# Kernel optimization log

Measured on AMD Instinct MI355X. Metric: run time of the kernel, lower is better.

The kernel has to match this reference:

```python
import jax, jax.numpy as jnp
import numpy as np

DIM = 256
FOCAL_LEVEL = 3
FOCAL_WINDOW = 3
FOCAL_FACTOR = 2


def _dwconv(x, k):
    # depthwise conv, SAME padding via explicit k//2 (matches ZeroPadding2D + VALID Conv2D)
    p = k.shape[0] // 2
    return jax.lax.conv_general_dilated(
        x, k, window_strides=(1, 1), padding=[(p, p), (p, p)],
        dimension_numbers=("NHWC", "HWIO", "NHWC"), feature_group_count=DIM)


def setup_inputs() -> dict:
    key = jax.random.key(0)
    ks = jax.random.split(key, 8)
    B, H, W = 32, 64, 64
    C_out = 2 * DIM + (FOCAL_LEVEL + 1)  # 516
    x = jax.random.normal(ks[0], (B, H, W, DIM), jnp.float32)
    w_init = jax.random.normal(ks[1], (DIM, C_out), jnp.float32) * 0.02
    b_init = jnp.zeros((C_out,), jnp.float32)
    kernels = []
    for i in range(FOCAL_LEVEL):
        s = FOCAL_FACTOR * i + FOCAL_WINDOW  # 3, 5, 7
        kernels.append(jax.random.normal(ks[2 + i], (s, s, 1, DIM), jnp.float32) * 0.02)
    w_mod = jax.random.normal(ks[5], (DIM, DIM), jnp.float32) * 0.02
    b_mod = jnp.zeros((DIM,), jnp.float32)
    w_proj = jax.random.normal(ks[6], (DIM, DIM), jnp.float32) * 0.02
    b_proj = jnp.zeros((DIM,), jnp.float32)
    return {"x": x, "w_init": w_init, "b_init": b_init,
            "k0": kernels[0], "k1": kernels[1], "k2": kernels[2],
            "w_mod": w_mod, "b_mod": b_mod, "w_proj": w_proj, "b_proj": b_proj}


def reference(x, w_init, b_init, k0, k1, k2, w_mod, b_mod, w_proj, b_proj):
    gelu = lambda t: jax.nn.gelu(t, approximate=False)
    x_proj = x @ w_init + b_init                       # [B,H,W,2*DIM+L+1]
    query = x_proj[..., :DIM]
    context = x_proj[..., DIM:2 * DIM]
    gates = jnp.clip(x_proj[..., 2 * DIM:], -1.0, 1.0)  # [B,H,W,L+1]

    ctx = gelu(_dwconv(context, k0))
    context_all = ctx * gates[..., 0:1]
    for idx, k in enumerate((k1, k2), start=1):
        ctx = gelu(_dwconv(ctx, k))
        context_all = context_all + ctx * gates[..., idx:idx + 1]

    context_global = jnp.tanh(jnp.mean(ctx, axis=(1, 2), keepdims=True))  # GAP+tanh
    context_all = context_all + context_global * gates[..., FOCAL_LEVEL:]

    modulator = context_all @ w_mod + b_mod            # 1x1 conv == per-pixel dense
    query = jnp.clip(query, -100.0, 100.0)
    modulator = jnp.clip(modulator, -100.0, 100.0)
    out = (query * modulator) @ w_proj + b_proj        # dropout identity (eval)
    return out
```

## Files before the change

### kernel.cpp

```cpp
#include <hip/hip_runtime.h>
#include <math.h>

#define DIMC 256
#define CO   516
#define NB   32
#define NH   64
#define NW   64
#define NPIX (NB*NH*NW)
#define PITCH 264
#define CP    76
#define CROWS 72

typedef short short8 __attribute__((ext_vector_type(8)));
typedef float floatx4 __attribute__((ext_vector_type(4)));
typedef unsigned short us4 __attribute__((ext_vector_type(4)));

__device__ __forceinline__ float gelu_f(float x) {
    return 0.5f * x * (1.0f + erff(x * 0.7071067811865476f));
}
__device__ __forceinline__ float clip100(float v) {
    return fminf(100.f, fmaxf(-100.f, v));
}
__device__ __forceinline__ void split2(float x, unsigned short& h, unsigned short& l) {
    unsigned int xb = __float_as_uint(x);
    unsigned int hb = (xb + 0x7fffu + ((xb >> 16) & 1u)) & 0xffff0000u;
    h = (unsigned short)(hb >> 16);
    float r = x - __uint_as_float(hb);
    unsigned int rb = __float_as_uint(r);
    l = (unsigned short)((rb + 0x7fffu + ((rb >> 16) & 1u)) >> 16);
}

__global__ __launch_bounds__(256) void k_prep(const float* __restrict__ w_init,
                                              const float* __restrict__ w_mod,
                                              const float* __restrict__ w_proj,
                                              unsigned short* wiF_h, unsigned short* wiF_l,
                                              unsigned short* wmF_h, unsigned short* wmF_l,
                                              unsigned short* wpF_h, unsigned short* wpF_l,
                                              unsigned short* wgF_h, unsigned short* wgF_l) {
    const int n = blockIdx.x;
    const int k = threadIdx.x;
    const int kki = k >> 5, quad = (k >> 3) & 3, j = k & 7;
    unsigned short h, l;
    if (n < 1024) {
        const int nn = (n < 512) ? n : (n < 768 ? n - 512 : n - 768);
        const int g = nn >> 6, in_ = (nn >> 4) & 3, l15 = nn & 15;
        const size_t idx = ((size_t)((g * 8 + kki) * 4 + in_) * 64 + quad * 16 + l15) * 8 + j;
        if (n < 512) {
            split2(w_init[k * CO + n], h, l);
            wiF_h[idx] = h; wiF_l[idx] = l;
        } else if (n < 768) {
            split2(w_mod[k * 256 + nn], h, l);
            wmF_h[idx] = h; wmF_l[idx] = l;
        } else {
            split2(w_proj[k * 256 + nn], h, l);
            wpF_h[idx] = h; wpF_l[idx] = l;
        }
    } else {
        const int nn = n - 1024;
        const float v = (nn < 4) ? w_init[k * CO + 512 + nn] : 0.f;
        split2(v, h, l);
        const size_t idx = ((size_t)kki * 64 + quad * 16 + nn) * 8 + j;
        wgF_h[idx] = h; wgF_l[idx] = l;
    }
}

__global__ __launch_bounds__(256) void k_init_mfma(const float* __restrict__ x,
                                                   const unsigned short* __restrict__ wiF_h,
                                                   const unsigned short* __restrict__ wiF_l,
                                                   const unsigned short* __restrict__ wgF_h,
                                                   const unsigned short* __restrict__ wgF_l,
                                                   const float* __restrict__ b_init,
                                                   float* __restrict__ qout,
                                                   float* __restrict__ ctxp,
                                                   float* __restrict__ gates) {
    __shared__ unsigned short Ah[8192];
    __shared__ unsigned short Al[8192];
    const int t = threadIdx.x;
    const int wv = t >> 6, lane = t & 63;
    const int l15 = lane & 15, quad = lane >> 4;
    const long tile = blockIdx.x;
    const long p0 = tile * 64;
    const int bb = (int)(p0 >> 12);
    const int pl = (int)(p0 & 4095);

    const float* xr = x + (size_t)(p0 + wv * 16 + l15) * 256 + quad * 8;
    const unsigned short* BqH = wiF_h + (size_t)wv * 16384;
    const unsigned short* BqL = wiF_l + (size_t)wv * 16384;
    const unsigned short* BcH = wiF_h + (size_t)(4 + wv) * 16384;
    const unsigned short* BcL = wiF_l + (size_t)(4 + wv) * 16384;

    floatx4 accq[4][4], accc[4][4], gacc;
    #pragma unroll
    for (int im = 0; im < 4; ++im)
        #pragma unroll
        for (int in_ = 0; in_ < 4; ++in_) {
            accq[im][in_] = (floatx4){0.f, 0.f, 0.f, 0.f};
            accc[im][in_] = (floatx4){0.f, 0.f, 0.f, 0.f};
        }
    gacc = (floatx4){0.f, 0.f, 0.f, 0.f};

    #pragma unroll
    for (int h = 0; h < 2; ++h) {
        #pragma unroll
        for (int kk2 = 0; kk2 < 4; ++kk2) {
            const int kki = h * 4 + kk2;
            const float4 v0 = *(const float4*)&xr[kki * 32];
            const float4 v1 = *(const float4*)&xr[kki * 32 + 4];
            short8 hh, ll;
            unsigned short hs, ls;
            split2(v0.x, hs, ls); hh[0] = (short)hs; ll[0] = (short)ls;
            split2(v0.y, hs, ls); hh[1] = (short)hs; ll[1] = (short)ls;
            split2(v0.z, hs, ls); hh[2] = (short)hs; ll[2] = (short)ls;
            split2(v0.w, hs, ls); hh[3] = (short)hs; ll[3] = (short)ls;
            split2(v1.x, hs, ls); hh[4] = (short)hs; ll[4] = (short)ls;
            split2(v1.y, hs, ls); hh[5] = (short)hs; ll[5] = (short)ls;
            split2(v1.z, hs, ls); hh[6] = (short)hs; ll[6] = (short)ls;
            split2(v1.w, hs, ls); hh[7] = (short)hs; ll[7] = (short)ls;
            const int o = ((wv * 4 + kk2) * 64 + lane) * 8;
            *(short8*)&Ah[o] = hh;
            *(short8*)&Al[o] = ll;
        }
        __syncthreads();

        #pragma unroll
        for (int kk2 = 0; kk2 < 4; ++kk2) {
            const int kki = h * 4 + kk2;
            short8 ah[4], al[4], bh[4], bl[4];
            #pragma unroll
            for (int im = 0; im < 4; ++im) {
                const int o = ((im * 4 + kk2) * 64 + lane) * 8;
                ah[im] = *(const short8*)&Ah[o];
                al[im] = *(const short8*)&Al[o];
            }
            #pragma unroll
            for (int in_ = 0; in_ < 4; ++in_) {
                const int o = ((kki * 4 + in_) * 64 + lane) * 8;
                bh[in_] = *(const short8*)&BqH[o];
                bl[in_] = *(const short8*)&BqL[o];
            }
            #pragma unroll
            for (int im = 0; im < 4; ++im)
                #pragma unroll
                for (int in_ = 0; in_ < 4; ++in_) {
                    accq[im][in_] = __builtin_amdgcn_mfma_f32_16x16x32_bf16(ah[im], bh[in_], accq[im][in_], 0, 0, 0);
                    accq[im][in_] = __builtin_amdgcn_mfma_f32_16x16x32_bf16(ah[im], bl[in_], accq[im][in_], 0, 0, 0);
                    accq[im][in_] = __builtin_amdgcn_mfma_f32_16x16x32_bf16(al[im], bh[in_], accq[im][in_], 0, 0, 0);
                }
            #pragma unroll
            for (int in_ = 0; in_ < 4; ++in_) {
                const int o = ((kki * 4 + in_) * 64 + lane) * 8;
                bh[in_] = *(const short8*)&BcH[o];
                bl[in_] = *(const short8*)&BcL[o];
            }
            #pragma unroll
            for (int im = 0; im < 4; ++im)
                #pragma unroll
                for (int in_ = 0; in_ < 4; ++in_) {
                    accc[im][in_] = __builtin_amdgcn_mfma_f32_16x16x32_bf16(ah[im], bh[in_], accc[im][in_], 0, 0, 0);
                    accc[im][in_] = __builtin_amdgcn_mfma_f32_16x16x32_bf16(ah[im], bl[in_], accc[im][in_], 0, 0, 0);
                    accc[im][in_] = __builtin_amdgcn_mfma_f32_16x16x32_bf16(al[im], bh[in_], accc[im][in_], 0, 0, 0);
                }
            {
                const int oga = ((wv * 4 + kk2) * 64 + lane) * 8;
                const short8 gah = *(const short8*)&Ah[oga];
                const short8 gal = *(const short8*)&Al[oga];
                const int ob = (kki * 64 + lane) * 8;
                const short8 gbh = *(const short8*)&wgF_h[ob];
                const short8 gbl = *(const short8*)&wgF_l[ob];
                gacc = __builtin_amdgcn_mfma_f32_16x16x32_bf16(gah, gbh, gacc, 0, 0, 0);
                gacc = __builtin_amdgcn_mfma_f32_16x16x32_bf16(gah, gbl, gacc, 0, 0, 0);
                gacc = __builtin_amdgcn_mfma_f32_16x16x32_bf16(gal, gbh, gacc, 0, 0, 0);
            }
        }
        if (h == 0) __syncthreads();
    }

    #pragma unroll
    for (int in_ = 0; in_ < 4; ++in_) {
        const int col = wv * 64 + in_ * 16 + l15;
        const float bi = b_init[col];
        #pragma unroll
        for (int im = 0; im < 4; ++im)
            #pragma unroll
            for (int r = 0; r < 4; ++r) {
                const int row = im * 16 + quad * 4 + r;
                qout[(p0 + row) * 256 + col] = accq[im][in_][r] + bi;
            }
    }
    #pragma unroll
    for (int in_ = 0; in_ < 4; ++in_) {
        const int col = wv * 64 + in_ * 16 + l15;
        const float bi = b_init[256 + col];
        #pragma unroll
        for (int im = 0; im < 4; ++im) {
            float4 o;
            o.x = accc[im][in_][0] + bi;
            o.y = accc[im][in_][1] + bi;
            o.z = accc[im][in_][2] + bi;
            o.w = accc[im][in_][3] + bi;
            *(float4*)&ctxp[((size_t)bb * 256 + col) * 4096 + pl + im * 16 + quad * 4] = o;
        }
    }
    if (l15 < 4) {
        const float bi = b_init[512 + l15];
        #pragma unroll
        for (int r = 0; r < 4; ++r) {
            const int row = wv * 16 + quad * 4 + r;
            gates[(p0 + row) * 4 + l15] = fminf(1.f, fmaxf(-1.f, gacc[r] + bi));
        }
    }
}

template<int KS>
__device__ __forceinline__ void conv_level(const float* __restrict__ kwp,
                                           const float* __restrict__ I,
                                           int ry0, int cx0, float v[8]) {
    constexpr int P = KS / 2;
    constexpr int RWIN = 2 + 2 * P;
    float wk[KS * KS];
    #pragma unroll
    for (int i = 0; i < KS * KS; ++i) wk[i] = kwp[i * 256];

    float4 rb[RWIN][3];
    #pragma unroll
    for (int r = 0; r < 2 * P; ++r) {
        const int base = (ry0 + r - P + 4) * CP + cx0;
        rb[r][0] = *(const float4*)&I[base];
        rb[r][1] = *(const float4*)&I[base + 4];
        rb[r][2] = *(const float4*)&I[base + 8];
    }
    #pragma unroll
    for (int j = 0; j < 2; ++j) {
        {
            const int r = j + 2 * P;
            const int base = (ry0 + r - P + 4) * CP + cx0;
            rb[r][0] = *(const float4*)&I[base];
            rb[r][1] = *(const float4*)&I[base + 4];
            rb[r][2] = *(const float4*)&I[base + 8];
        }
        float s0 = 0.f, s1 = 0.f, s2 = 0.f, s3 = 0.f;
        #pragma unroll
        for (int dy = 0; dy < KS; ++dy) {
            const float* rw = (const float*)&rb[j + dy][0];
            #pragma unroll
            for (int dx = 0; dx < KS; ++dx) {
                const float wgt = wk[dy * KS + dx];
                s0 += rw[4 - P + 0 + dx] * wgt;
                s1 += rw[4 - P + 1 + dx] * wgt;
                s2 += rw[4 - P + 2 + dx] * wgt;
                s3 += rw[4 - P + 3 + dx] * wgt;
            }
        }
        v[j * 4 + 0] = gelu_f(s0);
        v[j * 4 + 1] = gelu_f(s1);
        v[j * 4 + 2] = gelu_f(s2);
        v[j * 4 + 3] = gelu_f(s3);
    }
}

__global__ __launch_bounds__(512) void k_conv_fused(const float* __restrict__ ctxp,
                                                    const float* __restrict__ k0,
                                                    const float* __restrict__ k1,
                                                    const float* __restrict__ k2,
                                                    const float* __restrict__ gates,
                                                    float* __restrict__ c_allp) {
    __shared__ float X[CROWS * CP];
    __shared__ float Y[CROWS * CP];
    const int t = threadIdx.x;
    const int bc = blockIdx.x;
    const int b = bc >> 8, c = bc & 255;
    const float* src = ctxp + (size_t)bc * 4096;

    for (int i = t; i < CROWS * CP; i += 512) { X[i] = 0.f; Y[i] = 0.f; }
    __syncthreads();
    #pragma unroll
    for (int i = 0; i < 2; ++i) {
        const int p = i * 2048 + t * 4;
        const float4 vv = *(const float4*)&src[p];
        *(float4*)&X[((p >> 6) + 4) * CP + (p & 63) + 4] = vv;
    }
    __syncthreads();

    const int px = t & 15, py = t >> 4;
    const int cx0 = px * 4, ry0 = py * 2;
    const float* gbase = gates + (size_t)b * 4096 * 4;

    float acc[8], v[8];

    conv_level<3>(k0 + c, X, ry0, cx0, v);
    #pragma unroll
    for (int j = 0; j < 2; ++j) {
        *(float4*)&Y[(ry0 + j + 4) * CP + cx0 + 4] = *(float4*)&v[j * 4];
        #pragma unroll
        for (int i2 = 0; i2 < 4; ++i2)
            acc[j * 4 + i2] = v[j * 4 + i2] * gbase[((ry0 + j) * 64 + cx0 + i2) * 4 + 0];
    }
    __syncthreads();

    conv_level<5>(k1 + c, Y, ry0, cx0, v);
    #pragma unroll
    for (int j = 0; j < 2; ++j) {
        *(float4*)&X[(ry0 + j + 4) * CP + cx0 + 4] = *(float4*)&v[j * 4];
        #pragma unroll
        for (int i2 = 0; i2 < 4; ++i2)
            acc[j * 4 + i2] += v[j * 4 + i2] * gbase[((ry0 + j) * 64 + cx0 + i2) * 4 + 1];
    }
    __syncthreads();

    conv_level<7>(k2 + c, X, ry0, cx0, v);
    float vsum = 0.f;
    #pragma unroll
    for (int j = 0; j < 2; ++j)
        #pragma unroll
        for (int i2 = 0; i2 < 4; ++i2) {
            acc[j * 4 + i2] += v[j * 4 + i2] * gbase[((ry0 + j) * 64 + cx0 + i2) * 4 + 2];
            vsum += v[j * 4 + i2];
        }

    __syncthreads();
    X[t] = vsum;
    __syncthreads();
    if (t < 64) {
        float s = 0.f;
        #pragma unroll
        for (int k = 0; k < 8; ++k) s += X[t + 64 * k];
        #pragma unroll
        for (int off = 32; off >= 1; off >>= 1)
            s += __shfl_down(s, off, 64);
        if (t == 0) X[0] = tanhf(s * (1.f / 4096.f));
    }
    __syncthreads();
    const float gl = X[0];

    float* dst = c_allp + (size_t)bc * 4096;
    #pragma unroll
    for (int j = 0; j < 2; ++j) {
        float4 o;
        o.x = acc[j * 4 + 0] + gl * gbase[((ry0 + j) * 64 + cx0 + 0) * 4 + 3];
        o.y = acc[j * 4 + 1] + gl * gbase[((ry0 + j) * 64 + cx0 + 1) * 4 + 3];
        o.z = acc[j * 4 + 2] + gl * gbase[((ry0 + j) * 64 + cx0 + 2) * 4 + 3];
        o.w = acc[j * 4 + 3] + gl * gbase[((ry0 + j) * 64 + cx0 + 3) * 4 + 3];
        *(float4*)&dst[(ry0 + j) * 64 + cx0] = o;
    }
}

__global__ __launch_bounds__(256) void k_final_mfma(float* qout,
                                                    const float* __restrict__ c_allp,
                                                    const unsigned short* __restrict__ wmF_h,
                                                    const unsigned short* __restrict__ wmF_l,
                                                    const unsigned short* __restrict__ wpF_h,
                                                    const unsigned short* __restrict__ wpF_l,
                                                    const float* __restrict__ b_mod,
                                                    const float* __restrict__ b_proj) {
    __shared__ unsigned short Ah[64 * PITCH];
    __shared__ unsigned short Al[64 * PITCH];
    const int t = threadIdx.x;
    const long p0 = (long)blockIdx.x * 64;
    const int b = (int)(p0 >> 12);
    const int pl = (int)(p0 & 4095);

    {
        const float* src = c_allp + ((size_t)b * 256 + t) * 4096 + pl;
        #pragma unroll
        for (int i = 0; i < 16; ++i) {
            const float4 vv = *(const float4*)&src[i * 4];
            unsigned short h, l;
            split2(vv.x, h, l); Ah[(i*4+0)*PITCH + t] = h; Al[(i*4+0)*PITCH + t] = l;
            split2(vv.y, h, l); Ah[(i*4+1)*PITCH + t] = h; Al[(i*4+1)*PITCH + t] = l;
            split2(vv.z, h, l); Ah[(i*4+2)*PITCH + t] = h; Al[(i*4+2)*PITCH + t] = l;
            split2(vv.w, h, l); Ah[(i*4+3)*PITCH + t] = h; Al[(i*4+3)*PITCH + t] = l;
        }
    }
    __syncthreads();

    const int wv = t >> 6, lane = t & 63;
    const int l15 = lane & 15, quad = lane >> 4;
    const int ncol0 = wv * 64;
    const unsigned short* BmH = wmF_h + (size_t)wv * 16384;
    const unsigned short* BmL = wmF_l + (size_t)wv * 16384;
    const unsigned short* BpH = wpF_h + (size_t)wv * 16384;
    const unsigned short* BpL = wpF_l + (size_t)wv * 16384;

    floatx4 acc[4][4];
    #pragma unroll
    for (int im = 0; im < 4; ++im)
        #pragma unroll
        for (int in_ = 0; in_ < 4; ++in_)
            acc[im][in_] = (floatx4){0.f, 0.f, 0.f, 0.f};

    #pragma unroll
    for (int kki = 0; kki < 8; ++kki) {
        short8 ah[4], al[4], bh[4], bl[4];
        #pragma unroll
        for (int in_ = 0; in_ < 4; ++in_) {
            const int o = ((kki * 4 + in_) * 64 + lane) * 8;
            bh[in_] = *(const short8*)&BmH[o];
            bl[in_] = *(const short8*)&BmL[o];
        }
        #pragma unroll
        for (int im = 0; im < 4; ++im) {
            const int off = (im * 16 + l15) * PITCH + kki * 32 + quad * 8;
            ah[im] = *(const short8*)&Ah[off];
            al[im] = *(const short8*)&Al[off];
        }
        #pragma unroll
        for (int im = 0; im < 4; ++im)
            #pragma unroll
            for (int in_ = 0; in_ < 4; ++in_) {
                acc[im][in_] = __builtin_amdgcn_mfma_f32_16x16x32_bf16(ah[im], bh[in_], acc[im][in_], 0, 0, 0);
                acc[im][in_] = __builtin_amdgcn_mfma_f32_16x16x32_bf16(ah[im], bl[in_], acc[im][in_], 0, 0, 0);
                acc[im][in_] = __builtin_amdgcn_mfma_f32_16x16x32_bf16(al[im], bh[in_], acc[im][in_], 0, 0, 0);
            }
    }
    __syncthreads();

    #pragma unroll
    for (int in_ = 0; in_ < 4; ++in_) {
        const int col = ncol0 + in_ * 16 + l15;
        const float bm = b_mod[col];
        #pragma unroll
        for (int im = 0; im < 4; ++im)
            #pragma unroll
            for (int r = 0; r < 4; ++r) {
                const int row = im * 16 + quad * 4 + r;
                const float m = clip100(acc[im][in_][r] + bm);
                const float qv = clip100(qout[(p0 + row) * 256 + col]);
                unsigned short h, l;
                split2(qv * m, h, l);
                Ah[row * PITCH + col] = h;
                Al[row * PITCH + col] = l;
            }
    }
    __syncthreads();

    #pragma unroll
    for (int im = 0; im < 4; ++im)
        #pragma unroll
        for (int in_ = 0; in_ < 4; ++in_)
            acc[im][in_] = (floatx4){0.f, 0.f, 0.f, 0.f};

    #pragma unroll
    for (int kki = 0; kki < 8; ++kki) {
        short8 ah[4], al[4], bh[4], bl[4];
        #pragma unroll
        for (int in_ = 0; in_ < 4; ++in_) {
            const int o = ((kki * 4 + in_) * 64 + lane) * 8;
            bh[in_] = *(const short8*)&BpH[o];
            bl[in_] = *(const short8*)&BpL[o];
        }
        #pragma unroll
        for (int im = 0; im < 4; ++im) {
            const int off = (im * 16 + l15) * PITCH + kki * 32 + quad * 8;
            ah[im] = *(const short8*)&Ah[off];
            al[im] = *(const short8*)&Al[off];
        }
        #pragma unroll
        for (int im = 0; im < 4; ++im)
            #pragma unroll
            for (int in_ = 0; in_ < 4; ++in_) {
                acc[im][in_] = __builtin_amdgcn_mfma_f32_16x16x32_bf16(ah[im], bh[in_], acc[im][in_], 0, 0, 0);
                acc[im][in_] = __builtin_amdgcn_mfma_f32_16x16x32_bf16(ah[im], bl[in_], acc[im][in_], 0, 0, 0);
                acc[im][in_] = __builtin_amdgcn_mfma_f32_16x16x32_bf16(al[im], bh[in_], acc[im][in_], 0, 0, 0);
            }
    }

    #pragma unroll
    for (int in_ = 0; in_ < 4; ++in_) {
        const int col = ncol0 + in_ * 16 + l15;
        const float bp = b_proj[col];
        #pragma unroll
        for (int im = 0; im < 4; ++im)
            #pragma unroll
            for (int r = 0; r < 4; ++r) {
                const int row = im * 16 + quad * 4 + r;
                qout[(p0 + row) * 256 + col] = acc[im][in_][r] + bp;
            }
    }
}

extern "C" void kernel_launch(void* const* d_in, const int* in_sizes, int n_in,
                              void* d_out, int out_size, void* d_ws, size_t ws_size,
                              hipStream_t stream) {
    const float* x      = (const float*)d_in[0];
    const float* w_init = (const float*)d_in[1];
    const float* b_init = (const float*)d_in[2];
    const float* k0     = (const float*)d_in[3];
    const float* k1     = (const float*)d_in[4];
    const float* k2     = (const float*)d_in[5];
    const float* w_mod  = (const float*)d_in[6];
    const float* b_mod  = (const float*)d_in[7];
    const float* w_proj = (const float*)d_in[8];
    const float* b_proj = (const float*)d_in[9];
    float* qout = (float*)d_out;

    float* ws = (float*)d_ws;
    const long NP = (long)NPIX * DIMC;
    float* ctxp    = ws;
    float* c_allp  = ws + NP;
    float* gates   = ws + 2 * NP;
    unsigned short* wiF_h = (unsigned short*)(gates + (long)NPIX * 4);
    unsigned short* wiF_l = wiF_h + 512 * 256;
    unsigned short* wmF_h = wiF_l + 512 * 256;
    unsigned short* wmF_l = wmF_h + 256 * 256;
    unsigned short* wpF_h = wmF_l + 256 * 256;
    unsigned short* wpF_l = wpF_h + 256 * 256;
    unsigned short* wgF_h = wpF_l + 256 * 256;
    unsigned short* wgF_l = wgF_h + 16 * 256;

    k_prep<<<1040, 256, 0, stream>>>(w_init, w_mod, w_proj,
                                     wiF_h, wiF_l, wmF_h, wmF_l, wpF_h, wpF_l,
                                     wgF_h, wgF_l);
    k_init_mfma<<<NPIX / 64, 256, 0, stream>>>(x, wiF_h, wiF_l,
                                               wgF_h, wgF_l, b_init,
                                               qout, ctxp, gates);
    k_conv_fused<<<NB * 256, 512, 0, stream>>>(ctxp, k0, k1, k2, gates, c_allp);
    k_final_mfma<<<NPIX / 64, 256, 0, stream>>>(qout, c_allp,
                                                wmF_h, wmF_l, wpF_h, wpF_l,
                                                b_mod, b_proj);
}
```

Measured before the change: 866.0 us.

## Store gates planar per batch, stream conv rows, zero only halo

Gates are now written in a planar [B,4,H*W] layout, so the depthwise conv kernel reads them as coalesced float4 loads instead of strided scalar loads. The conv inner routine streams each input row once and accumulates both output rows from it, which removes the register row buffer and the preloaded weight array. Only the halo border of the shared buffers is zeroed, and a separate small shared array is used for the reduction. Weights are now reloaded from global memory inside the loop, which adds redundant loads that may or may not be served from cache.

Result: faster. 836.7 us (-3.4%).

```diff
diff --git a/kernel.cpp b/kernel.cpp
--- a/kernel.cpp
+++ b/kernel.cpp
@@ -13,7 +13,6 @@
 
 typedef short short8 __attribute__((ext_vector_type(8)));
 typedef float floatx4 __attribute__((ext_vector_type(4)));
-typedef unsigned short us4 __attribute__((ext_vector_type(4)));
 
 __device__ __forceinline__ float gelu_f(float x) {
     return 0.5f * x * (1.0f + erff(x * 0.7071067811865476f));
@@ -72,7 +71,7 @@
                                                    const float* __restrict__ b_init,
                                                    float* __restrict__ qout,
                                                    float* __restrict__ ctxp,
-                                                   float* __restrict__ gates) {
+                                                   float* __restrict__ gatesp) {
     __shared__ unsigned short Ah[8192];
     __shared__ unsigned short Al[8192];
     const int t = threadIdx.x;
@@ -206,7 +205,8 @@
         #pragma unroll
         for (int r = 0; r < 4; ++r) {
             const int row = wv * 16 + quad * 4 + r;
-            gates[(p0 + row) * 4 + l15] = fminf(1.f, fmaxf(-1.f, gacc[r] + bi));
+            gatesp[((size_t)bb * 4 + l15) * 4096 + pl + row] =
+                fminf(1.f, fmaxf(-1.f, gacc[r] + bi));
         }
     }
 }
@@ -216,62 +216,65 @@
                                            const float* __restrict__ I,
                                            int ry0, int cx0, float v[8]) {
     constexpr int P = KS / 2;
-    constexpr int RWIN = 2 + 2 * P;
-    float wk[KS * KS];
-    #pragma unroll
-    for (int i = 0; i < KS * KS; ++i) wk[i] = kwp[i * 256];
-
-    float4 rb[RWIN][3];
-    #pragma unroll
-    for (int r = 0; r < 2 * P; ++r) {
+    float a0[4] = {0.f, 0.f, 0.f, 0.f};
+    float a1[4] = {0.f, 0.f, 0.f, 0.f};
+    #pragma unroll
+    for (int r = 0; r < 2 * P + 2; ++r) {
         const int base = (ry0 + r - P + 4) * CP + cx0;
-        rb[r][0] = *(const float4*)&I[base];
-        rb[r][1] = *(const float4*)&I[base + 4];
-        rb[r][2] = *(const float4*)&I[base + 8];
-    }
-    #pragma unroll
-    for (int j = 0; j < 2; ++j) {
-        {
-            const int r = j + 2 * P;
-            const int base = (ry0 + r - P + 4) * CP + cx0;
-            rb[r][0] = *(const float4*)&I[base];
-            rb[r][1] = *(const float4*)&I[base + 4];
-            rb[r][2] = *(const float4*)&I[base + 8];
-        }
-        float s0 = 0.f, s1 = 0.f, s2 = 0.f, s3 = 0.f;
-        #pragma unroll
-        for (int dy = 0; dy < KS; ++dy) {
-            const float* rw = (const float*)&rb[j + dy][0];
+        const float4 w0 = *(const float4*)&I[base];
+        const float4 w1 = *(const float4*)&I[base + 4];
+        const float4 w2 = *(const float4*)&I[base + 8];
+        float rw[12] = {w0.x, w0.y, w0.z, w0.w,
+                        w1.x, w1.y, w1.z, w1.w,
+                        w2.x, w2.y, w2.z, w2.w};
+        if (r <= 2 * P) {
             #pragma unroll
             for (int dx = 0; dx < KS; ++dx) {
-                const float wgt = wk[dy * KS + dx];
-                s0 += rw[4 - P + 0 + dx] * wgt;
-                s1 += rw[4 - P + 1 + dx] * wgt;
-                s2 += rw[4 - P + 2 + dx] * wgt;
-                s3 += rw[4 - P + 3 + dx] * wgt;
-            }
-        }
-        v[j * 4 + 0] = gelu_f(s0);
-        v[j * 4 + 1] = gelu_f(s1);
-        v[j * 4 + 2] = gelu_f(s2);
-        v[j * 4 + 3] = gelu_f(s3);
-    }
+                const float wg = kwp[(r * KS + dx) * 256];
+                a0[0] += rw[4 - P + 0 + dx] * wg;
+                a0[1] += rw[4 - P + 1 + dx] * wg;
+                a0[2] += rw[4 - P + 2 + dx] * wg;
+                a0[3] += rw[4 - P + 3 + dx] * wg;
+            }
+        }
+        if (r >= 1) {
+            #pragma unroll
+            for (int dx = 0; dx < KS; ++dx) {
+                const float wg = kwp[((r - 1) * KS + dx) * 256];
+                a1[0] += rw[4 - P + 0 + dx] * wg;
+                a1[1] += rw[4 - P + 1 + dx] * wg;
+                a1[2] += rw[4 - P + 2 + dx] * wg;
+                a1[3] += rw[4 - P + 3 + dx] * wg;
+            }
+        }
+    }
+    v[0] = gelu_f(a0[0]); v[1] = gelu_f(a0[1]); v[2] = gelu_f(a0[2]); v[3] = gelu_f(a0[3]);
+    v[4] = gelu_f(a1[0]); v[5] = gelu_f(a1[1]); v[6] = gelu_f(a1[2]); v[7] = gelu_f(a1[3]);
 }
 
 __global__ __launch_bounds__(512) void k_conv_fused(const float* __restrict__ ctxp,
                                                     const float* __restrict__ k0,
                                                     const float* __restrict__ k1,
                                                     const float* __restrict__ k2,
-                                                    const float* __restrict__ gates,
+                                                    const float* __restrict__ gatesp,
                                                     float* __restrict__ c_allp) {
     __shared__ float X[CROWS * CP];
     __shared__ float Y[CROWS * CP];
+    __shared__ float S[512];
     const int t = threadIdx.x;
     const int bc = blockIdx.x;
     const int b = bc >> 8, c = bc & 255;
     const float* src = ctxp + (size_t)bc * 4096;
 
-    for (int i = t; i < CROWS * CP; i += 512) { X[i] = 0.f; Y[i] = 0.f; }
+    for (int i = t; i < 4 * CP; i += 512) {
+        X[i] = 0.f; X[68 * CP + i] = 0.f;
+        Y[i] = 0.f; Y[68 * CP + i] = 0.f;
+    }
+    for (int i = t; i < 64 * 12; i += 512) {
+        const int r = i / 12, cc = i % 12;
+        const int off = (r + 4) * CP + (cc < 4 ? cc : cc + 64);
+        X[off] = 0.f; Y[off] = 0.f;
+    }
     __syncthreads();
     #pragma unroll
     for (int i = 0; i < 2; ++i) {
@@ -283,64 +286,70 @@
 
     const int px = t & 15, py = t >> 4;
     const int cx0 = px * 4, ry0 = py * 2;
-    const float* gbase = gates + (size_t)b * 4096 * 4;
+    const float* gp0 = gatesp + ((size_t)b * 4 + 0) * 4096;
+    const float* gp1 = gatesp + ((size_t)b * 4 + 1) * 4096;
+    const float* gp2 = gatesp + ((size_t)b * 4 + 2) * 4096;
+    const float* gp3 = gatesp + ((size_t)b * 4 + 3) * 4096;
 
     float acc[8], v[8];
 
-    conv_level<3>(k0 + c, X, ry0, cx0, v);
-    #pragma unroll
-    for (int j = 0; j < 2; ++j) {
-        *(float4*)&Y[(ry0 + j + 4) * CP + cx0 + 4] = *(float4*)&v[j * 4];
-        #pragma unroll
-        for (int i2 = 0; i2 < 4; ++i2)
-            acc[j * 4 + i2] = v[j * 4 + i2] * gbase[((ry0 + j) * 64 + cx0 + i2) * 4 + 0];
-    }
-    __syncthreads();
-
-    conv_level<5>(k1 + c, Y, ry0, cx0, v);
-    #pragma unroll
-    for (int j = 0; j < 2; ++j) {
-        *(float4*)&X[(ry0 + j + 4) * CP + cx0 + 4] = *(float4*)&v[j * 4];
-        #pragma unroll
-        for (int i2 = 0; i2 < 4; ++i2)
-            acc[j * 4 + i2] += v[j * 4 + i2] * gbase[((ry0 + j) * 64 + cx0 + i2) * 4 + 1];
-    }
-    __syncthreads();
-
-    conv_level<7>(k2 + c, X, ry0, cx0, v);
-    float vsum = 0.f;
-    #pragma unroll
-    for (int j = 0; j < 2; ++j)
-        #pragma unroll
-        for (int i2 = 0; i2 < 4; ++i2) {
-            acc[j * 4 + i2] += v[j * 4 + i2] * gbase[((ry0 + j) * 64 + cx0 + i2) * 4 + 2];
-            vsum += v[j * 4 + i2];
-        }
-
-    __syncthreads();
-    X[t] = vsum;
+    {
+        const float4 ga = *(const float4*)&gp0[(ry0 + 0) * 64 + cx0];
+        const float4 gb = *(const float4*)&gp0[(ry0 + 1) * 64 + cx0];
+        conv_level<3>(k0 + c, X, ry0, cx0, v);
+        *(float4*)&Y[(ry0 + 4) * CP + cx0 + 4] = *(float4*)&v[0];
+        *(float4*)&Y[(ry0 + 5) * CP + cx0 + 4] = *(float4*)&v[4];
+        acc[0] = v[0] * ga.x; acc[1] = v[1] * ga.y; acc[2] = v[2] * ga.z; acc[3] = v[3] * ga.w;
+        acc[4] = v[4] * gb.x; acc[5] = v[5] * gb.y; acc[6] = v[6] * gb.z; acc[7] = v[7] * gb.w;
+    }
+    __syncthreads();
+
+    {
+        const float4 ga = *(const float4*)&gp1[(ry0 + 0) * 64 + cx0];
+        const float4 gb = *(const float4*)&gp1[(ry0 + 1) * 64 + cx0];
+        conv_level<5>(k1 + c, Y, ry0, cx0, v);
+        *(float4*)&X[(ry0 + 4) * CP + cx0 + 4] = *(float4*)&v[0];
+        *(float4*)&X[(ry0 + 5) * CP + cx0 + 4] = *(float4*)&v[4];
+        acc[0] += v[0] * ga.x; acc[1] += v[1] * ga.y; acc[2] += v[2] * ga.z; acc[3] += v[3] * ga.w;
+        acc[4] += v[4] * gb.x; acc[5] += v[5] * gb.y; acc[6] += v[6] * gb.z; acc[7] += v[7] * gb.w;
+    }
+    __syncthreads();
+
+    float vsum;
+    {
+        const float4 ga = *(const float4*)&gp2[(ry0 + 0) * 64 + cx0];
+        const float4 gb = *(const float4*)&gp2[(ry0 + 1) * 64 + cx0];
+        conv_level<7>(k2 + c, X, ry0, cx0, v);
+        acc[0] += v[0] * ga.x; acc[1] += v[1] * ga.y; acc[2] += v[2] * ga.z; acc[3] += v[3] * ga.w;
+        acc[4] += v[4] * gb.x; acc[5] += v[5] * gb.y; acc[6] += v[6] * gb.z; acc[7] += v[7] * gb.w;
+        vsum = v[0] + v[1] + v[2] + v[3] + v[4] + v[5] + v[6] + v[7];
+    }
+
+    S[t] = vsum;
     __syncthreads();
     if (t < 64) {
         float s = 0.f;
         #pragma unroll
-        for (int k = 0; k < 8; ++k) s += X[t + 64 * k];
+        for (int k = 0; k < 8; ++k) s += S[t + 64 * k];
         #pragma unroll
         for (int off = 32; off >= 1; off >>= 1)
             s += __shfl_down(s, off, 64);
-        if (t == 0) X[0] = tanhf(s * (1.f / 4096.f));
-    }
-    __syncthreads();
-    const float gl = X[0];
+        if (t == 0) S[0] = tanhf(s * (1.f / 4096.f));
+    }
+    __syncthreads();
+    const float gl = S[0];
 
     float* dst = c_allp + (size_t)bc * 4096;
-    #pragma unroll
-    for (int j = 0; j < 2; ++j) {
-        float4 o;
-        o.x = acc[j * 4 + 0] + gl * gbase[((ry0 + j) * 64 + cx0 + 0) * 4 + 3];
-        o.y = acc[j * 4 + 1] + gl * gbase[((ry0 + j) * 64 + cx0 + 1) * 4 + 3];
-        o.z = acc[j * 4 + 2] + gl * gbase[((ry0 + j) * 64 + cx0 + 2) * 4 + 3];
-        o.w = acc[j * 4 + 3] + gl * gbase[((ry0 + j) * 64 + cx0 + 3) * 4 + 3];
-        *(float4*)&dst[(ry0 + j) * 64 + cx0] = o;
+    {
+        const float4 ga = *(const float4*)&gp3[(ry0 + 0) * 64 + cx0];
+        const float4 gb = *(const float4*)&gp3[(ry0 + 1) * 64 + cx0];
+        float4 o0, o1;
+        o0.x = acc[0] + gl * ga.x; o0.y = acc[1] + gl * ga.y;
+        o0.z = acc[2] + gl * ga.z; o0.w = acc[3] + gl * ga.w;
+        o1.x = acc[4] + gl * gb.x; o1.y = acc[5] + gl * gb.y;
+        o1.z = acc[6] + gl * gb.z; o1.w = acc[7] + gl * gb.w;
+        *(float4*)&dst[(ry0 + 0) * 64 + cx0] = o0;
+        *(float4*)&dst[(ry0 + 1) * 64 + cx0] = o1;
     }
 }
 
@@ -497,8 +506,8 @@
     const long NP = (long)NPIX * DIMC;
     float* ctxp    = ws;
     float* c_allp  = ws + NP;
-    float* gates   = ws + 2 * NP;
-    unsigned short* wiF_h = (unsigned short*)(gates + (long)NPIX * 4);
+    float* gatesp  = ws + 2 * NP;
+    unsigned short* wiF_h = (unsigned short*)(gatesp + (long)NPIX * 4);
     unsigned short* wiF_l = wiF_h + 512 * 256;
     unsigned short* wmF_h = wiF_l + 512 * 256;
     unsigned short* wmF_l = wmF_h + 256 * 256;
@@ -512,8 +521,8 @@
                                      wgF_h, wgF_l);
     k_init_mfma<<<NPIX / 64, 256, 0, stream>>>(x, wiF_h, wiF_l,
                                                wgF_h, wgF_l, b_init,
-                                               qout, ctxp, gates);
-    k_conv_fused<<<NB * 256, 512, 0, stream>>>(ctxp, k0, k1, k2, gates, c_allp);
+                                               qout, ctxp, gatesp);
+    k_conv_fused<<<NB * 256, 512, 0, stream>>>(ctxp, k0, k1, k2, gatesp, c_allp);
     k_final_mfma<<<NPIX / 64, 256, 0, stream>>>(qout, c_allp,
                                                 wmF_h, wmF_l, wpF_h, wpF_l,
                                                 b_mod, b_proj);
```
